# Performance work log

Hardware: AMD Instinct MI355X
Metric: run time of the kernel (lower is better)

The kernel has to match this reference:

```python
import jax, jax.numpy as jnp
import numpy as np

TOP_K = 2
SCALING = 32.0 / 16.0  # alpha / rank


def setup_inputs() -> dict:
    key = jax.random.key(0)
    ks = jax.random.split(key, 8)
    B_, S, D = 4, 4096, 2048
    E, R, H = 5, 16, 256
    return {
        "x": jax.random.normal(ks[0], (B_, S, D), jnp.float32),
        "base_output": jax.random.normal(ks[1], (B_, S, D), jnp.float32),
        "A": jax.random.normal(ks[2], (E, D, R), jnp.float32) * (1.0 / R),
        "B": jax.random.normal(ks[3], (E, R, D), jnp.float32) * 0.02,
        "W1": jax.random.normal(ks[4], (D, H), jnp.float32) * (1.0 / np.sqrt(D)),
        "b1": jnp.zeros((H,), jnp.float32),
        "W2": jax.random.normal(ks[5], (H, E), jnp.float32) * (1.0 / np.sqrt(H)),
        "b2": jnp.zeros((E,), jnp.float32),
    }


def reference(x, base_output, A, B, W1, b1, W2, b2):
    # Router: Linear -> SiLU -> Linear -> softmax
    routing_logits = jax.nn.silu(x @ W1 + b1) @ W2 + b2          # [B,S,E]
    routing_weights = jax.nn.softmax(routing_logits, axis=-1)
    top_k_weights, top_k_indices = jax.lax.top_k(routing_weights, TOP_K)  # [B,S,K]
    top_k_weights = top_k_weights / top_k_weights.sum(-1, keepdims=True)

    # Dense per-expert LoRA eval (faithful to original): x @ A_e @ B_e * scaling
    low = jnp.einsum('bsd,edr->bser', x, A)                       # [B,S,E,R]
    expert_outputs = jnp.einsum('bser,erd->bsed', low, B) * SCALING  # [B,S,E,D]

    # Gather selected experts and combine with normalized weights
    gathered = jnp.take_along_axis(expert_outputs, top_k_indices[..., None], axis=2)  # [B,S,K,D]
    combined = (gathered * top_k_weights[..., None]).sum(axis=2)  # [B,S,D]
    return base_output + combined
```

## Files before the change

kernel.cpp:

```cpp
#include <hip/hip_runtime.h>
#include <math.h>

#define N_TOK 16384
#define D_DIM 2048
#define H_DIM 256
#define E_NUM 5
#define R_DIM 16
#define ER 80

#define NCT 21
#define KSTEPS 32

typedef _Float16 half8 __attribute__((ext_vector_type(8)));
typedef float f32x4 __attribute__((ext_vector_type(4)));

__global__ __launch_bounds__(256) void pack_w_kernel(
    const float* __restrict__ W1, const float* __restrict__ A,
    _Float16* __restrict__ Whi, _Float16* __restrict__ Wlo,
    float* __restrict__ logits) {
  const int idx = blockIdx.x * 256 + threadIdx.x;
  if (idx < N_TOK * E_NUM) logits[idx] = 0.f;
  const int lane = idx & 63;
  const int kgct = idx >> 6;
  const int kg = kgct & 63;
  const int ct = kgct >> 6;
  const int k0 = kg * 32 + ((lane >> 4) << 3);
  const int par = lane & 15;
  float v[8];
  if (ct < 16) {
    const int col = ct * 16 + par;
#pragma unroll
    for (int j = 0; j < 8; ++j) v[j] = W1[(size_t)(k0 + j) * H_DIM + col];
  } else {
    const float* Ae = A + (size_t)(ct - 16) * D_DIM * R_DIM;
#pragma unroll
    for (int j = 0; j < 8; ++j) v[j] = Ae[(size_t)(k0 + j) * R_DIM + par];
  }
  half8 hv, lv;
#pragma unroll
  for (int j = 0; j < 8; ++j) {
    const _Float16 hh = (_Float16)v[j];
    hv[j] = hh;
    lv[j] = (_Float16)(v[j] - (float)hh);
  }
  ((half8*)Whi)[(size_t)kgct * 64 + lane] = hv;
  ((half8*)Wlo)[(size_t)kgct * 64 + lane] = lv;
}

__global__ __launch_bounds__(256, 3) void xgemm_kernel(
    const float* __restrict__ x, const float* __restrict__ b1,
    const _Float16* __restrict__ Whi, const _Float16* __restrict__ Wlo,
    const float* __restrict__ W2, float* __restrict__ logits,
    float* __restrict__ P) {
  __shared__ _Float16 lds[2][2][8][64][8];
  __shared__ float w2s[H_DIM * E_NUM];
  const int t = threadIdx.x;
  const int tok0 = blockIdx.x * 64;
  const int y = blockIdx.y;
  const int lane = t & 63;
  const int w = t >> 6;
  const int sr = t >> 2;
  const int q = t & 3;
  const int lq = lane >> 4;
  const int lp = lane & 15;

  const float* xrow = x + (size_t)(tok0 + sr) * D_DIM + (q << 4);

  {
    float xv[16];
    *(float4*)&xv[0] = *(const float4*)(xrow);
    *(float4*)&xv[4] = *(const float4*)(xrow + 4);
    *(float4*)&xv[8] = *(const float4*)(xrow + 8);
    *(float4*)&xv[12] = *(const float4*)(xrow + 12);
#pragma unroll
    for (int hf = 0; hf < 2; ++hf) {
      half8 hv, lv;
#pragma unroll
      for (int j = 0; j < 8; ++j) {
        const float v = xv[(hf << 3) + j];
        const _Float16 hh = (_Float16)v;
        hv[j] = hh;
        lv[j] = (_Float16)(v - (float)hh);
      }
      const int kq = (q << 1) + hf;
      *(half8*)&lds[0][0][kq][sr ^ kq][0] = hv;
      *(half8*)&lds[0][1][kq][sr ^ kq][0] = lv;
    }
  }

  const half8* WH = (const half8*)Whi;
  const half8* WL = (const half8*)Wlo;

  if (y < 2) {
    f32x4 acc[4][2];
#pragma unroll
    for (int i = 0; i < 4; ++i)
#pragma unroll
      for (int j = 0; j < 2; ++j) acc[i][j] = (f32x4)0.f;
    const int ctg0 = (y << 3) + (w << 1);
    int cur = 0;
    for (int kg = 0; kg < KSTEPS; ++kg) {
      __syncthreads();
      float xv[16];
      const bool more = (kg < KSTEPS - 1);
      if (more) {
        const float* src = xrow + (kg + 1) * 64;
        *(float4*)&xv[0] = *(const float4*)(src);
        *(float4*)&xv[4] = *(const float4*)(src + 4);
        *(float4*)&xv[8] = *(const float4*)(src + 8);
        *(float4*)&xv[12] = *(const float4*)(src + 12);
      }
      half8 bh[2][2], bl[2][2];
#pragma unroll
      for (int ct = 0; ct < 2; ++ct)
#pragma unroll
        for (int h2 = 0; h2 < 2; ++h2) {
          const size_t wo = ((size_t)(ctg0 + ct) * 64 + (kg << 1) + h2) * 64 + lane;
          bh[ct][h2] = WH[wo];
          bl[ct][h2] = WL[wo];
        }
#pragma unroll
      for (int h2 = 0; h2 < 2; ++h2) {
        const int kq = (h2 << 2) + lq;
#pragma unroll
        for (int rt = 0; rt < 4; ++rt) {
          const int r = ((rt << 4) + lp) ^ kq;
          const half8 ah = *(const half8*)&lds[cur][0][kq][r][0];
          const half8 al = *(const half8*)&lds[cur][1][kq][r][0];
#pragma unroll
          for (int ct = 0; ct < 2; ++ct) {
            acc[rt][ct] = __builtin_amdgcn_mfma_f32_16x16x32_f16(al, bh[ct][h2], acc[rt][ct], 0, 0, 0);
            acc[rt][ct] = __builtin_amdgcn_mfma_f32_16x16x32_f16(ah, bl[ct][h2], acc[rt][ct], 0, 0, 0);
            acc[rt][ct] = __builtin_amdgcn_mfma_f32_16x16x32_f16(ah, bh[ct][h2], acc[rt][ct], 0, 0, 0);
          }
        }
      }
      if (more) {
#pragma unroll
        for (int hf = 0; hf < 2; ++hf) {
          half8 hv, lv;
#pragma unroll
          for (int j = 0; j < 8; ++j) {
            const float v = xv[(hf << 3) + j];
            const _Float16 hh = (_Float16)v;
            hv[j] = hh;
            lv[j] = (_Float16)(v - (float)hh);
          }
          const int kq = (q << 1) + hf;
          *(half8*)&lds[cur ^ 1][0][kq][sr ^ kq][0] = hv;
          *(half8*)&lds[cur ^ 1][1][kq][sr ^ kq][0] = lv;
        }
      }
      cur ^= 1;
    }
    for (int i = t; i < H_DIM * E_NUM; i += 256) w2s[i] = W2[i];
    __syncthreads();
    const int colb = (y << 7) + (w << 5);
#pragma unroll
    for (int rt = 0; rt < 4; ++rt) {
      float pl[4][5];
#pragma unroll
      for (int rg = 0; rg < 4; ++rg)
#pragma unroll
        for (int e = 0; e < 5; ++e) pl[rg][e] = 0.f;
#pragma unroll
      for (int ct = 0; ct < 2; ++ct) {
        const int col = colb + (ct << 4) + lp;
        const float bb = b1[col];
        float w2c[5];
#pragma unroll
        for (int e = 0; e < 5; ++e) w2c[e] = w2s[col * 5 + e];
#pragma unroll
        for (int rg = 0; rg < 4; ++rg) {
          float v = acc[rt][ct][rg] + bb;
          v = v / (1.f + expf(-v));
#pragma unroll
          for (int e = 0; e < 5; ++e) pl[rg][e] = fmaf(v, w2c[e], pl[rg][e]);
        }
      }
#pragma unroll
      for (int m = 1; m < 16; m <<= 1)
#pragma unroll
        for (int rg = 0; rg < 4; ++rg)
#pragma unroll
          for (int e = 0; e < 5; ++e) pl[rg][e] += __shfl_xor(pl[rg][e], m, 64);
      if (lp == 0) {
        const int row0 = tok0 + (rt << 4) + (lq << 2);
#pragma unroll
        for (int rg = 0; rg < 4; ++rg)
#pragma unroll
          for (int e = 0; e < 5; ++e)
            atomicAdd(&logits[(size_t)(row0 + rg) * E_NUM + e], pl[rg][e]);
      }
    }
  } else {
    f32x4 acc[5];
#pragma unroll
    for (int j = 0; j < 5; ++j) acc[j] = (f32x4)0.f;
    int cur = 0;
    for (int kg = 0; kg < KSTEPS; ++kg) {
      __syncthreads();
      float xv[16];
      const bool more = (kg < KSTEPS - 1);
      if (more) {
        const float* src = xrow + (kg + 1) * 64;
        *(float4*)&xv[0] = *(const float4*)(src);
        *(float4*)&xv[4] = *(const float4*)(src + 4);
        *(float4*)&xv[8] = *(const float4*)(src + 8);
        *(float4*)&xv[12] = *(const float4*)(src + 12);
      }
      half8 bh[5][2], bl[5][2];
#pragma unroll
      for (int ct = 0; ct < 5; ++ct)
#pragma unroll
        for (int h2 = 0; h2 < 2; ++h2) {
          const size_t wo = ((size_t)(16 + ct) * 64 + (kg << 1) + h2) * 64 + lane;
          bh[ct][h2] = WH[wo];
          bl[ct][h2] = WL[wo];
        }
#pragma unroll
      for (int h2 = 0; h2 < 2; ++h2) {
        const int kq = (h2 << 2) + lq;
        const int r = ((w << 4) + lp) ^ kq;
        const half8 ah = *(const half8*)&lds[cur][0][kq][r][0];
        const half8 al = *(const half8*)&lds[cur][1][kq][r][0];
#pragma unroll
        for (int ct = 0; ct < 5; ++ct) {
          acc[ct] = __builtin_amdgcn_mfma_f32_16x16x32_f16(al, bh[ct][h2], acc[ct], 0, 0, 0);
          acc[ct] = __builtin_amdgcn_mfma_f32_16x16x32_f16(ah, bl[ct][h2], acc[ct], 0, 0, 0);
          acc[ct] = __builtin_amdgcn_mfma_f32_16x16x32_f16(ah, bh[ct][h2], acc[ct], 0, 0, 0);
        }
      }
      if (more) {
#pragma unroll
        for (int hf = 0; hf < 2; ++hf) {
          half8 hv, lv;
#pragma unroll
          for (int j = 0; j < 8; ++j) {
            const float v = xv[(hf << 3) + j];
            const _Float16 hh = (_Float16)v;
            hv[j] = hh;
            lv[j] = (_Float16)(v - (float)hh);
          }
          const int kq = (q << 1) + hf;
          *(half8*)&lds[cur ^ 1][0][kq][sr ^ kq][0] = hv;
          *(half8*)&lds[cur ^ 1][1][kq][sr ^ kq][0] = lv;
        }
      }
      cur ^= 1;
    }
#pragma unroll
    for (int ct = 0; ct < 5; ++ct)
#pragma unroll
      for (int rg = 0; rg < 4; ++rg) {
        const int row = tok0 + (w << 4) + (lq << 2) + rg;
        P[(size_t)row * ER + (ct << 4) + lp] = acc[ct][rg];
      }
  }
}

__global__ __launch_bounds__(256) void combine_kernel(
    const float* __restrict__ P, const float* __restrict__ Bm,
    const float* __restrict__ base, const float* __restrict__ logits,
    const float* __restrict__ b2, float* __restrict__ out) {
  __shared__ float Pl[64][80];
  __shared__ float sc[64][5];
  const int t = threadIdx.x;
  const int wg = __builtin_amdgcn_readfirstlane(t >> 6);
  const int c4 = ((blockIdx.x & 7) << 8) + ((t & 63) << 2);
  const int tokb = (blockIdx.x >> 3) << 6;

  if (t < 64) {
    float lg[5];
#pragma unroll
    for (int e = 0; e < 5; ++e)
      lg[e] = logits[(size_t)(tokb + t) * E_NUM + e] + b2[e];
    int e0 = 0;
#pragma unroll
    for (int e = 1; e < 5; ++e) if (lg[e] > lg[e0]) e0 = e;
    int e1 = (e0 == 0) ? 1 : 0;
#pragma unroll
    for (int e = 0; e < 5; ++e) if (e != e0 && lg[e] > lg[e1]) e1 = e;
    const float qq = expf(lg[e1] - lg[e0]);
    const float s0 = 2.f / (1.f + qq);
    const float s1 = qq * s0;
#pragma unroll
    for (int e = 0; e < 5; ++e)
      sc[t][e] = (e == e0) ? s0 : ((e == e1) ? s1 : 0.f);
  }
  __syncthreads();
  {
    const int row = t >> 2;
    const int off = (t & 3) * 20;
    const float* prow = P + (size_t)(tokb + row) * ER + off;
#pragma unroll
    for (int j = 0; j < 5; ++j) {
      float4 v = *(const float4*)(prow + (j << 2));
      v.x *= sc[row][(off + (j << 2) + 0) >> 4];
      v.y *= sc[row][(off + (j << 2) + 1) >> 4];
      v.z *= sc[row][(off + (j << 2) + 2) >> 4];
      v.w *= sc[row][(off + (j << 2) + 3) >> 4];
      *(float4*)&Pl[row][off + (j << 2)] = v;
    }
  }
  __syncthreads();

  float4 acc[16];
#pragma unroll
  for (int i = 0; i < 16; ++i) acc[i] = make_float4(0.f, 0.f, 0.f, 0.f);
  const int r0 = wg << 4;

  for (int k0 = 0; k0 < ER; k0 += 4) {
    const float4 bv0 = *(const float4*)(Bm + (size_t)(k0 + 0) * D_DIM + c4);
    const float4 bv1 = *(const float4*)(Bm + (size_t)(k0 + 1) * D_DIM + c4);
    const float4 bv2 = *(const float4*)(Bm + (size_t)(k0 + 2) * D_DIM + c4);
    const float4 bv3 = *(const float4*)(Bm + (size_t)(k0 + 3) * D_DIM + c4);
#pragma unroll
    for (int i = 0; i < 16; ++i) {
      float pv[4];
      *(float4*)pv = *(const float4*)&Pl[r0 + i][k0];
      acc[i].x = fmaf(pv[0], bv0.x, fmaf(pv[1], bv1.x, fmaf(pv[2], bv2.x, fmaf(pv[3], bv3.x, acc[i].x))));
      acc[i].y = fmaf(pv[0], bv0.y, fmaf(pv[1], bv1.y, fmaf(pv[2], bv2.y, fmaf(pv[3], bv3.y, acc[i].y))));
      acc[i].z = fmaf(pv[0], bv0.z, fmaf(pv[1], bv1.z, fmaf(pv[2], bv2.z, fmaf(pv[3], bv3.z, acc[i].z))));
      acc[i].w = fmaf(pv[0], bv0.w, fmaf(pv[1], bv1.w, fmaf(pv[2], bv2.w, fmaf(pv[3], bv3.w, acc[i].w))));
    }
  }

#pragma unroll
  for (int i = 0; i < 16; ++i) {
    const size_t o = (size_t)(tokb + r0 + i) * D_DIM + c4;
    const float4 b = *(const float4*)(base + o);
    float4 r;
    r.x = acc[i].x + b.x;
    r.y = acc[i].y + b.y;
    r.z = acc[i].z + b.z;
    r.w = acc[i].w + b.w;
    *(float4*)(out + o) = r;
  }
}

extern "C" void kernel_launch(void* const* d_in, const int* in_sizes, int n_in,
                              void* d_out, int out_size, void* d_ws,
                              size_t ws_size, hipStream_t stream) {
  const float* x  = (const float*)d_in[0];
  const float* bo = (const float*)d_in[1];
  const float* A  = (const float*)d_in[2];
  const float* Bm = (const float*)d_in[3];
  const float* W1 = (const float*)d_in[4];
  const float* b1 = (const float*)d_in[5];
  const float* W2 = (const float*)d_in[6];
  const float* b2 = (const float*)d_in[7];
  float* out = (float*)d_out;

  char* ws = (char*)d_ws;
  float* P = (float*)ws;
  _Float16* Whi = (_Float16*)(ws + 5242880);
  _Float16* Wlo = (_Float16*)(ws + 5242880 + 1376256);
  float* logits = (float*)(ws + 5242880 + 2 * 1376256);

  pack_w_kernel<<<336, 256, 0, stream>>>(W1, A, Whi, Wlo, logits);
  xgemm_kernel<<<dim3(N_TOK / 64, 3), 256, 0, stream>>>(x, b1, Whi, Wlo, W2,
                                                        logits, P);
  combine_kernel<<<(N_TOK / 64) * (D_DIM / 256), 256, 0, stream>>>(
      P, Bm, bo, logits, b2, out);
}
```

Before: 476.5 us.

## Software-pipeline weight loads and replace logit atomics with per-block partial sums

The GEMM loop now splits each K step into even and odd halves and prefetches the next half's packed weights while the current half's MFMAs run, so global weight latency is hidden. Router logits are reduced across waves in shared memory and written as two per-y partial arrays, which removes global atomics and the zero-init in the pack kernel. The combine kernel sums the partials, preloads base_output into its accumulators before the routing work, and sets an occupancy hint. The cost is more live registers for the prefetched weights and extra workspace for the partial logits.

```diff
diff --git a/kernel.cpp b/kernel.cpp
--- a/kernel.cpp
+++ b/kernel.cpp
@@ -16,10 +16,8 @@
 
 __global__ __launch_bounds__(256) void pack_w_kernel(
     const float* __restrict__ W1, const float* __restrict__ A,
-    _Float16* __restrict__ Whi, _Float16* __restrict__ Wlo,
-    float* __restrict__ logits) {
+    _Float16* __restrict__ Whi, _Float16* __restrict__ Wlo) {
   const int idx = blockIdx.x * 256 + threadIdx.x;
-  if (idx < N_TOK * E_NUM) logits[idx] = 0.f;
   const int lane = idx & 63;
   const int kgct = idx >> 6;
   const int kg = kgct & 63;
@@ -50,10 +48,11 @@
 __global__ __launch_bounds__(256, 3) void xgemm_kernel(
     const float* __restrict__ x, const float* __restrict__ b1,
     const _Float16* __restrict__ Whi, const _Float16* __restrict__ Wlo,
-    const float* __restrict__ W2, float* __restrict__ logits,
+    const float* __restrict__ W2, float* __restrict__ plog,
     float* __restrict__ P) {
   __shared__ _Float16 lds[2][2][8][64][8];
   __shared__ float w2s[H_DIM * E_NUM];
+  __shared__ float plbuf[4][64][E_NUM];
   const int t = threadIdx.x;
   const int tok0 = blockIdx.x * 64;
   const int y = blockIdx.y;
@@ -98,11 +97,26 @@
 #pragma unroll
       for (int j = 0; j < 2; ++j) acc[i][j] = (f32x4)0.f;
     const int ctg0 = (y << 3) + (w << 1);
+
+    half8 bhE[2], blE[2], bhO[2], blO[2];
+#pragma unroll
+    for (int ct = 0; ct < 2; ++ct) {
+      const size_t wo = ((size_t)(ctg0 + ct) * 64 + 0) * 64 + lane;
+      bhE[ct] = WH[wo];
+      blE[ct] = WL[wo];
+    }
+
     int cur = 0;
     for (int kg = 0; kg < KSTEPS; ++kg) {
       __syncthreads();
+      const bool more = (kg < KSTEPS - 1);
+#pragma unroll
+      for (int ct = 0; ct < 2; ++ct) {
+        const size_t wo = ((size_t)(ctg0 + ct) * 64 + (kg << 1) + 1) * 64 + lane;
+        bhO[ct] = WH[wo];
+        blO[ct] = WL[wo];
+      }
       float xv[16];
-      const bool more = (kg < KSTEPS - 1);
       if (more) {
         const float* src = xrow + (kg + 1) * 64;
         *(float4*)&xv[0] = *(const float4*)(src);
@@ -110,29 +124,37 @@
         *(float4*)&xv[8] = *(const float4*)(src + 8);
         *(float4*)&xv[12] = *(const float4*)(src + 12);
       }
-      half8 bh[2][2], bl[2][2];
-#pragma unroll
-      for (int ct = 0; ct < 2; ++ct)
-#pragma unroll
-        for (int h2 = 0; h2 < 2; ++h2) {
-          const size_t wo = ((size_t)(ctg0 + ct) * 64 + (kg << 1) + h2) * 64 + lane;
-          bh[ct][h2] = WH[wo];
-          bl[ct][h2] = WL[wo];
-        }
-#pragma unroll
-      for (int h2 = 0; h2 < 2; ++h2) {
-        const int kq = (h2 << 2) + lq;
-#pragma unroll
-        for (int rt = 0; rt < 4; ++rt) {
-          const int r = ((rt << 4) + lp) ^ kq;
-          const half8 ah = *(const half8*)&lds[cur][0][kq][r][0];
-          const half8 al = *(const half8*)&lds[cur][1][kq][r][0];
-#pragma unroll
-          for (int ct = 0; ct < 2; ++ct) {
-            acc[rt][ct] = __builtin_amdgcn_mfma_f32_16x16x32_f16(al, bh[ct][h2], acc[rt][ct], 0, 0, 0);
-            acc[rt][ct] = __builtin_amdgcn_mfma_f32_16x16x32_f16(ah, bl[ct][h2], acc[rt][ct], 0, 0, 0);
-            acc[rt][ct] = __builtin_amdgcn_mfma_f32_16x16x32_f16(ah, bh[ct][h2], acc[rt][ct], 0, 0, 0);
-          }
+#pragma unroll
+      for (int rt = 0; rt < 4; ++rt) {
+        const int r = ((rt << 4) + lp) ^ lq;
+        const half8 ah = *(const half8*)&lds[cur][0][lq][r][0];
+        const half8 al = *(const half8*)&lds[cur][1][lq][r][0];
+#pragma unroll
+        for (int ct = 0; ct < 2; ++ct) {
+          acc[rt][ct] = __builtin_amdgcn_mfma_f32_16x16x32_f16(al, bhE[ct], acc[rt][ct], 0, 0, 0);
+          acc[rt][ct] = __builtin_amdgcn_mfma_f32_16x16x32_f16(ah, blE[ct], acc[rt][ct], 0, 0, 0);
+          acc[rt][ct] = __builtin_amdgcn_mfma_f32_16x16x32_f16(ah, bhE[ct], acc[rt][ct], 0, 0, 0);
+        }
+      }
+      if (more) {
+#pragma unroll
+        for (int ct = 0; ct < 2; ++ct) {
+          const size_t wo = ((size_t)(ctg0 + ct) * 64 + (kg << 1) + 2) * 64 + lane;
+          bhE[ct] = WH[wo];
+          blE[ct] = WL[wo];
+        }
+      }
+#pragma unroll
+      for (int rt = 0; rt < 4; ++rt) {
+        const int kq = 4 + lq;
+        const int r = ((rt << 4) + lp) ^ kq;
+        const half8 ah = *(const half8*)&lds[cur][0][kq][r][0];
+        const half8 al = *(const half8*)&lds[cur][1][kq][r][0];
+#pragma unroll
+        for (int ct = 0; ct < 2; ++ct) {
+          acc[rt][ct] = __builtin_amdgcn_mfma_f32_16x16x32_f16(al, bhO[ct], acc[rt][ct], 0, 0, 0);
+          acc[rt][ct] = __builtin_amdgcn_mfma_f32_16x16x32_f16(ah, blO[ct], acc[rt][ct], 0, 0, 0);
+          acc[rt][ct] = __builtin_amdgcn_mfma_f32_16x16x32_f16(ah, bhO[ct], acc[rt][ct], 0, 0, 0);
         }
       }
       if (more) {
@@ -153,6 +175,7 @@
       }
       cur ^= 1;
     }
+
     for (int i = t; i < H_DIM * E_NUM; i += 256) w2s[i] = W2[i];
     __syncthreads();
     const int colb = (y << 7) + (w << 5);
@@ -185,23 +208,45 @@
 #pragma unroll
           for (int e = 0; e < 5; ++e) pl[rg][e] += __shfl_xor(pl[rg][e], m, 64);
       if (lp == 0) {
-        const int row0 = tok0 + (rt << 4) + (lq << 2);
+        const int rl0 = (rt << 4) + (lq << 2);
 #pragma unroll
         for (int rg = 0; rg < 4; ++rg)
 #pragma unroll
-          for (int e = 0; e < 5; ++e)
-            atomicAdd(&logits[(size_t)(row0 + rg) * E_NUM + e], pl[rg][e]);
-      }
+          for (int e = 0; e < 5; ++e) plbuf[w][rl0 + rg][e] = pl[rg][e];
+      }
+    }
+    __syncthreads();
+    for (int i = t; i < 64 * E_NUM; i += 256) {
+      const int row = i / E_NUM;
+      const int e = i - row * E_NUM;
+      const float s = plbuf[0][row][e] + plbuf[1][row][e] +
+                      plbuf[2][row][e] + plbuf[3][row][e];
+      plog[((size_t)y * N_TOK + tok0 + row) * E_NUM + e] = s;
     }
   } else {
     f32x4 acc[5];
 #pragma unroll
     for (int j = 0; j < 5; ++j) acc[j] = (f32x4)0.f;
+
+    half8 bhE[5], blE[5], bhO[5], blO[5];
+#pragma unroll
+    for (int ct = 0; ct < 5; ++ct) {
+      const size_t wo = ((size_t)(16 + ct) * 64 + 0) * 64 + lane;
+      bhE[ct] = WH[wo];
+      blE[ct] = WL[wo];
+    }
+
     int cur = 0;
     for (int kg = 0; kg < KSTEPS; ++kg) {
       __syncthreads();
+      const bool more = (kg < KSTEPS - 1);
+#pragma unroll
+      for (int ct = 0; ct < 5; ++ct) {
+        const size_t wo = ((size_t)(16 + ct) * 64 + (kg << 1) + 1) * 64 + lane;
+        bhO[ct] = WH[wo];
+        blO[ct] = WL[wo];
+      }
       float xv[16];
-      const bool more = (kg < KSTEPS - 1);
       if (more) {
         const float* src = xrow + (kg + 1) * 64;
         *(float4*)&xv[0] = *(const float4*)(src);
@@ -209,26 +254,35 @@
         *(float4*)&xv[8] = *(const float4*)(src + 8);
         *(float4*)&xv[12] = *(const float4*)(src + 12);
       }
-      half8 bh[5][2], bl[5][2];
-#pragma unroll
-      for (int ct = 0; ct < 5; ++ct)
-#pragma unroll
-        for (int h2 = 0; h2 < 2; ++h2) {
-          const size_t wo = ((size_t)(16 + ct) * 64 + (kg << 1) + h2) * 64 + lane;
-          bh[ct][h2] = WH[wo];
-          bl[ct][h2] = WL[wo];
-        }
-#pragma unroll
-      for (int h2 = 0; h2 < 2; ++h2) {
-        const int kq = (h2 << 2) + lq;
+      {
+        const int r = ((w << 4) + lp) ^ lq;
+        const half8 ah = *(const half8*)&lds[cur][0][lq][r][0];
+        const half8 al = *(const half8*)&lds[cur][1][lq][r][0];
+#pragma unroll
+        for (int ct = 0; ct < 5; ++ct) {
+          acc[ct] = __builtin_amdgcn_mfma_f32_16x16x32_f16(al, bhE[ct], acc[ct], 0, 0, 0);
+          acc[ct] = __builtin_amdgcn_mfma_f32_16x16x32_f16(ah, blE[ct], acc[ct], 0, 0, 0);
+          acc[ct] = __builtin_amdgcn_mfma_f32_16x16x32_f16(ah, bhE[ct], acc[ct], 0, 0, 0);
+        }
+      }
+      if (more) {
+#pragma unroll
+        for (int ct = 0; ct < 5; ++ct) {
+          const size_t wo = ((size_t)(16 + ct) * 64 + (kg << 1) + 2) * 64 + lane;
+          bhE[ct] = WH[wo];
+          blE[ct] = WL[wo];
+        }
+      }
+      {
+        const int kq = 4 + lq;
         const int r = ((w << 4) + lp) ^ kq;
         const half8 ah = *(const half8*)&lds[cur][0][kq][r][0];
         const half8 al = *(const half8*)&lds[cur][1][kq][r][0];
 #pragma unroll
         for (int ct = 0; ct < 5; ++ct) {
-          acc[ct] = __builtin_amdgcn_mfma_f32_16x16x32_f16(al, bh[ct][h2], acc[ct], 0, 0, 0);
-          acc[ct] = __builtin_amdgcn_mfma_f32_16x16x32_f16(ah, bl[ct][h2], acc[ct], 0, 0, 0);
-          acc[ct] = __builtin_amdgcn_mfma_f32_16x16x32_f16(ah, bh[ct][h2], acc[ct], 0, 0, 0);
+          acc[ct] = __builtin_amdgcn_mfma_f32_16x16x32_f16(al, bhO[ct], acc[ct], 0, 0, 0);
+          acc[ct] = __builtin_amdgcn_mfma_f32_16x16x32_f16(ah, blO[ct], acc[ct], 0, 0, 0);
+          acc[ct] = __builtin_amdgcn_mfma_f32_16x16x32_f16(ah, bhO[ct], acc[ct], 0, 0, 0);
         }
       }
       if (more) {
@@ -259,9 +313,9 @@
   }
 }
 
-__global__ __launch_bounds__(256) void combine_kernel(
+__global__ __launch_bounds__(256, 4) void combine_kernel(
     const float* __restrict__ P, const float* __restrict__ Bm,
-    const float* __restrict__ base, const float* __restrict__ logits,
+    const float* __restrict__ base, const float* __restrict__ plog,
     const float* __restrict__ b2, float* __restrict__ out) {
   __shared__ float Pl[64][80];
   __shared__ float sc[64][5];
@@ -269,12 +323,19 @@
   const int wg = __builtin_amdgcn_readfirstlane(t >> 6);
   const int c4 = ((blockIdx.x & 7) << 8) + ((t & 63) << 2);
   const int tokb = (blockIdx.x >> 3) << 6;
+  const int r0 = wg << 4;
+
+  float4 acc[16];
+#pragma unroll
+  for (int i = 0; i < 16; ++i)
+    acc[i] = *(const float4*)(base + (size_t)(tokb + r0 + i) * D_DIM + c4);
 
   if (t < 64) {
+    const float* p0 = plog + (size_t)(tokb + t) * E_NUM;
+    const float* p1 = plog + ((size_t)N_TOK + tokb + t) * E_NUM;
     float lg[5];
 #pragma unroll
-    for (int e = 0; e < 5; ++e)
-      lg[e] = logits[(size_t)(tokb + t) * E_NUM + e] + b2[e];
+    for (int e = 0; e < 5; ++e) lg[e] = p0[e] + p1[e] + b2[e];
     int e0 = 0;
 #pragma unroll
     for (int e = 1; e < 5; ++e) if (lg[e] > lg[e0]) e0 = e;
@@ -305,11 +366,6 @@
   }
   __syncthreads();
 
-  float4 acc[16];
-#pragma unroll
-  for (int i = 0; i < 16; ++i) acc[i] = make_float4(0.f, 0.f, 0.f, 0.f);
-  const int r0 = wg << 4;
-
   for (int k0 = 0; k0 < ER; k0 += 4) {
     const float4 bv0 = *(const float4*)(Bm + (size_t)(k0 + 0) * D_DIM + c4);
     const float4 bv1 = *(const float4*)(Bm + (size_t)(k0 + 1) * D_DIM + c4);
@@ -329,13 +385,7 @@
 #pragma unroll
   for (int i = 0; i < 16; ++i) {
     const size_t o = (size_t)(tokb + r0 + i) * D_DIM + c4;
-    const float4 b = *(const float4*)(base + o);
-    float4 r;
-    r.x = acc[i].x + b.x;
-    r.y = acc[i].y + b.y;
-    r.z = acc[i].z + b.z;
-    r.w = acc[i].w + b.w;
-    *(float4*)(out + o) = r;
+    *(float4*)(out + o) = acc[i];
   }
 }
 
@@ -356,11 +406,11 @@
   float* P = (float*)ws;
   _Float16* Whi = (_Float16*)(ws + 5242880);
   _Float16* Wlo = (_Float16*)(ws + 5242880 + 1376256);
-  float* logits = (float*)(ws + 5242880 + 2 * 1376256);
-
-  pack_w_kernel<<<336, 256, 0, stream>>>(W1, A, Whi, Wlo, logits);
+  float* plog = (float*)(ws + 5242880 + 2 * 1376256);
+
+  pack_w_kernel<<<336, 256, 0, stream>>>(W1, A, Whi, Wlo);
   xgemm_kernel<<<dim3(N_TOK / 64, 3), 256, 0, stream>>>(x, b1, Whi, Wlo, W2,
-                                                        logits, P);
+                                                        plog, P);
   combine_kernel<<<(N_TOK / 64) * (D_DIM / 256), 256, 0, stream>>>(
-      P, Bm, bo, logits, b2, out);
+      P, Bm, bo, plog, b2, out);
 }
```

After: 822.0 us. 1.72x slower.
